# Performance work log

Measured on AMD Instinct MI355X. Metric: run time of the kernel, lower is better.

Reference implementation:

```python
import jax, jax.numpy as jnp
import numpy as np
import math

B, S, D, H = 2, 2048, 1024, 16
HD = D // H  # 64


def setup_inputs() -> dict:
    key = jax.random.key(0)
    ks = jax.random.split(key, 7)
    scale = 1.0 / math.sqrt(D)
    return {
        "hidden_states": jax.random.normal(ks[0], (B, S, D), jnp.float32),
        "attention_mask": jnp.zeros((B, 1, 1, S), jnp.int32),  # 0 = valid (code negates .bool())
        "Wq": jax.random.normal(ks[1], (D, D), jnp.float32) * scale,
        "bq": jnp.zeros((D,), jnp.float32),
        "Wk": jax.random.normal(ks[2], (D, D), jnp.float32) * scale,
        "bk": jnp.zeros((D,), jnp.float32),
        "Wv": jax.random.normal(ks[3], (D, D), jnp.float32) * scale,
        "bv": jnp.zeros((D,), jnp.float32),
    }


def reference(hidden_states, attention_mask, Wq, bq, Wk, bk, Wv, bv):
    b, s, d = hidden_states.shape

    def proj(W, bias):
        # torch Linear: x @ W.T + b ; weight shape [out, in]
        y = jnp.einsum('bsd,ed->bse', hidden_states, W) + bias
        return y.reshape(b, s, H, HD).transpose(0, 2, 1, 3)  # b h s d

    q, k, v = proj(Wq, bq), proj(Wk, bk), proj(Wv, bv)

    scores = jnp.einsum('bhqd,bhkd->bhqk', q, k) * (1.0 / math.sqrt(HD))
    causal = jnp.tril(jnp.ones((s, s), bool))[None, None]          # [1,1,S,S]
    pad = ~(attention_mask.astype(bool))                           # [B,1,1,S], True = valid
    mask = causal & pad
    scores = jnp.where(mask, scores, -jnp.inf)
    probs = jax.nn.softmax(scores, axis=-1)  # dropout prob = 0.0 -> identity
    out = jnp.einsum('bhqk,bhkd->bhqd', probs, v)
    return out.transpose(0, 2, 1, 3).reshape(b, s, d)
```

## Files before the change

### kernel.cpp

```cpp
#include <hip/hip_runtime.h>

typedef __bf16 bf16;
typedef __bf16 bf16x4 __attribute__((ext_vector_type(4)));
typedef __bf16 bf16x8 __attribute__((ext_vector_type(8)));
typedef float f32x4 __attribute__((ext_vector_type(4)));
typedef float f32x16 __attribute__((ext_vector_type(16)));
typedef unsigned u32x4 __attribute__((ext_vector_type(4)));

#define DEV __device__ __forceinline__

typedef const __attribute__((address_space(1))) void gvoid_t;
typedef __attribute__((address_space(3))) void lvoid_t;

DEV void gload_lds16(const void* g, void* l) {
  __builtin_amdgcn_global_load_lds((gvoid_t*)g, (lvoid_t*)l, 16, 0, 0);
}

DEV f32x4 mfma16(bf16x8 a, bf16x8 b, f32x4 c) {
  return __builtin_amdgcn_mfma_f32_16x16x32_bf16(a, b, c, 0, 0, 0);
}
DEV f32x16 mfma32(bf16x8 a, bf16x8 b, f32x16 c) {
  return __builtin_amdgcn_mfma_f32_32x32x16_bf16(a, b, c, 0, 0, 0);
}

DEV unsigned pk2(float lo, float hi) {
  unsigned r;
  asm("v_cvt_pk_bf16_f32 %0, %1, %2" : "=v"(r) : "v"(lo), "v"(hi));
  return r;
}

#define QSCALE 0.18033688011112042f

__global__ __launch_bounds__(256) void cvt_all(
    const float* __restrict__ hs, const float* __restrict__ Wq,
    const float* __restrict__ Wk, const float* __restrict__ Wv,
    bf16* __restrict__ Xb, bf16* __restrict__ Wb) {
  const int i = blockIdx.x * 256 + threadIdx.x;
  const float* src;
  bf16* dst;
  int off;
  if (i < 1048576) {
    src = hs; dst = Xb; off = i;
  } else {
    const int j = i - 1048576;
    const int sel = j >> 18;
    off = j & 262143;
    src = (sel == 0) ? Wq : (sel == 1) ? Wk : Wv;
    dst = Wb + (size_t)sel * 1048576;
  }
  float4 f = reinterpret_cast<const float4*>(src)[off];
  bf16x4 o;
  o[0] = (bf16)f.x; o[1] = (bf16)f.y; o[2] = (bf16)f.z; o[3] = (bf16)f.w;
  reinterpret_cast<bf16x4*>(dst)[off] = o;
}

__global__ __launch_bounds__(256) void gemm_qkv(
    const bf16* __restrict__ X, const bf16* __restrict__ W,
    const float* __restrict__ bq, const float* __restrict__ bk,
    const float* __restrict__ bv,
    bf16* __restrict__ Q, bf16* __restrict__ Kb, bf16* __restrict__ Vt) {
  __shared__ bf16 As[128 * 64];
  __shared__ bf16 Bs[128 * 64];
  const int t = threadIdx.x;
  const int lane = t & 63, w = t >> 6;
  const int wr = w >> 1, wc = w & 1;
  const int bid = blockIdx.x;
  const int swzb = (bid & 7) * 96 + (bid >> 3);
  const int m0 = (swzb / 24) * 128;
  const int n0 = (swzb % 24) * 128;
  const int cl = lane & 15, g8 = (lane >> 4) * 8;

  f32x4 acc[4][4];
  for (int mi = 0; mi < 4; ++mi)
    for (int ni = 0; ni < 4; ++ni)
      for (int r = 0; r < 4; ++r) acc[mi][ni][r] = 0.0f;

  for (int k0 = 0; k0 < 1024; k0 += 64) {
#pragma unroll
    for (int i = 0; i < 4; ++i) {
      int c = i * 256 + t;
      int row = c >> 3, col8 = (c & 7) * 8;
      gload_lds16(X + (size_t)(m0 + row) * 1024 + k0 + col8, As + c * 8);
      gload_lds16(W + (size_t)(n0 + row) * 1024 + k0 + col8, Bs + c * 8);
    }
    __syncthreads();
#pragma unroll
    for (int kk = 0; kk < 64; kk += 32) {
      bf16x8 a[4], b[4];
#pragma unroll
      for (int mi = 0; mi < 4; ++mi)
        a[mi] = *(const bf16x8*)&As[(wr * 64 + mi * 16 + cl) * 64 + kk + g8];
#pragma unroll
      for (int ni = 0; ni < 4; ++ni)
        b[ni] = *(const bf16x8*)&Bs[(wc * 64 + ni * 16 + cl) * 64 + kk + g8];
      __builtin_amdgcn_s_setprio(1);
#pragma unroll
      for (int mi = 0; mi < 4; ++mi)
#pragma unroll
        for (int ni = 0; ni < 4; ++ni)
          acc[mi][ni] = mfma16(a[mi], b[ni], acc[mi][ni]);
      __builtin_amdgcn_s_setprio(0);
    }
    __syncthreads();
  }

  const int rq = (lane >> 4) * 4;
#pragma unroll
  for (int mi = 0; mi < 4; ++mi) {
#pragma unroll
    for (int ni = 0; ni < 4; ++ni) {
      const int n = n0 + wc * 64 + ni * 16 + cl;
      const int mbase = m0 + wr * 64 + mi * 16 + rq;
      const int b = mbase >> 11, s0 = mbase & 2047;
      if (n < 1024) {
        const float bias = bq[n];
        const int h = n >> 6, hd = n & 63;
#pragma unroll
        for (int r = 0; r < 4; ++r)
          Q[(((size_t)(b * 16 + h)) * 2048 + s0 + r) * 64 + hd] =
              (bf16)((acc[mi][ni][r] + bias) * QSCALE);
      } else if (n < 2048) {
        const int n2 = n - 1024;
        const float bias = bk[n2];
        const int h = n2 >> 6, hd = n2 & 63;
#pragma unroll
        for (int r = 0; r < 4; ++r)
          Kb[(((size_t)(b * 16 + h)) * 2048 + s0 + r) * 64 + hd] =
              (bf16)(acc[mi][ni][r] + bias);
      } else {
        const int n2 = n - 2048;
        const float bias = bv[n2];
        const int h = n2 >> 6, hd = n2 & 63;
        bf16x4 pk;
#pragma unroll
        for (int r = 0; r < 4; ++r) pk[r] = (bf16)(acc[mi][ni][r] + bias);
        *(bf16x4*)&Vt[(((size_t)(b * 16 + h)) * 64 + hd) * 2048 + s0] = pk;
      }
    }
  }
}

__global__ __launch_bounds__(512, 4) void flash_attn(
    const bf16* __restrict__ Q, const bf16* __restrict__ K,
    const bf16* __restrict__ Vt, const int* __restrict__ amask,
    float* __restrict__ out) {
  __shared__ __align__(16) char arena[65536];
  __shared__ unsigned long long mk[32];
  bf16* Karena = (bf16*)arena;
  bf16* Varena = (bf16*)(arena + 32768);
  const int t = threadIdx.x, lane = t & 63, w = t >> 6;
  const int bh = blockIdx.x & 31;
  const int p = blockIdx.x >> 5;
  const int b = bh >> 4, h = bh & 15;
  const int g = w >> 1, par = w & 1;
  const int qt = (g < 2) ? (31 - p) : p;
  const int row0 = qt * 64 + (g & 1) * 32;
  const int r31 = lane & 31, hi = lane >> 5;
  const int swz = (r31 & 15) << 4;
  const int ntb = 32 - p;
  const int nsuper = (ntb + 1) >> 1;

  const bf16* Qp = Q + (size_t)bh * 2048 * 64;
  const bf16* Kp = K + (size_t)bh * 2048 * 64;
  const bf16* Vp = Vt + (size_t)bh * 64 * 2048;

  bf16x8 qf[4];
#pragma unroll
  for (int hdk = 0; hdk < 4; ++hdk)
    qf[hdk] = *(const bf16x8*)&Qp[(size_t)(row0 + r31) * 64 + hdk * 16 + hi * 8];

  f32x16 o[2];
#pragma unroll
  for (int hb = 0; hb < 2; ++hb)
#pragma unroll
    for (int rg = 0; rg < 16; ++rg) o[hb][rg] = 0.0f;
  float ls = 0.0f;

#pragma unroll
  for (int i = 0; i < 4; ++i) {
    const int kt = w * 4 + i;
    const unsigned long long bal =
        __ballot(amask[b * 2048 + kt * 64 + lane] != 0);
    if (lane == 0) mk[kt] = bal;
  }
#define STAGE(BIDX, KVB)                                                     \
  do {                                                                       \
    const int r_ = t >> 4, u_ = (t & 15) ^ (r_ & 15);                        \
    const int rr_ = (u_ >> 3) * 32 + r_, gb_ = (u_ & 7) * 8;                 \
    gload_lds16(Kp + (size_t)((KVB) + rr_) * 64 + gb_,                       \
                Karena + (BIDX)*4096 + t * 8);                               \
    gload_lds16(Vp + (size_t)rr_ * 2048 + (KVB) + gb_,                       \
                Varena + (BIDX)*4096 + t * 8);                               \
  } while (0)

  STAGE(0, 0);
  STAGE(1, 64);
  __syncthreads();

  for (int s = 0; s < nsuper; ++s) {
    const int pairbuf = s & 1;
    const int tn = 2 * s + 2;
    if (tn < ntb) STAGE((pairbuf ^ 1) * 2 + 0, tn * 64);
    if (tn + 1 < ntb) STAGE((pairbuf ^ 1) * 2 + 1, (tn + 1) * 64);
    const int kt = 2 * s + par;
    if (kt <= qt) {
      const int kv0 = kt * 64;
      const int bidx = pairbuf * 2 + par;
      const char* KtB = (const char*)(Karena + bidx * 4096);
      const char* VtB = (const char*)(Varena + bidx * 4096);
      const unsigned long long pb = mk[kt];
      const bool diag = (kt == qt);
      const bool domask = diag || (pb != 0ull);
#pragma unroll
      for (int half = 0; half < 2; ++half) {
        f32x16 s4;
#pragma unroll
        for (int rg = 0; rg < 16; ++rg) s4[rg] = -12.0f;
        __builtin_amdgcn_s_setprio(1);
#pragma unroll
        for (int hdk = 0; hdk < 4; ++hdk) {
          const bf16x8 kfr = *(const bf16x8*)(
              KtB + r31 * 256 + ((half * 128 + hdk * 32 + hi * 16) ^ swz));
          s4 = mfma32(kfr, qf[hdk], s4);
        }
        __builtin_amdgcn_s_setprio(0);
        if (domask) {
#pragma unroll
          for (int rg = 0; rg < 16; ++rg) {
            const int kvt = half * 32 + (rg & 3) + 8 * (rg >> 2) + 4 * hi;
            const bool bad = (diag && (kv0 + kvt > row0 + r31)) ||
                             ((pb >> kvt) & 1ull);
            s4[rg] = bad ? -1e30f : s4[rg];
          }
        }
        float pe[16];
#pragma unroll
        for (int rg = 0; rg < 16; ++rg) pe[rg] = exp2f(s4[rg]);
        ls += (((pe[0] + pe[1]) + (pe[2] + pe[3])) +
               ((pe[4] + pe[5]) + (pe[6] + pe[7]))) +
              (((pe[8] + pe[9]) + (pe[10] + pe[11])) +
               ((pe[12] + pe[13]) + (pe[14] + pe[15])));
#pragma unroll
        for (int j = 0; j < 2; ++j) {
          const unsigned a0 = pk2(pe[8 * j + 0], pe[8 * j + 1]);
          const unsigned a1 = pk2(pe[8 * j + 2], pe[8 * j + 3]);
          const unsigned b0 = pk2(pe[8 * j + 4], pe[8 * j + 5]);
          const unsigned b1 = pk2(pe[8 * j + 6], pe[8 * j + 7]);
          const unsigned xa0 = __shfl_xor(a0, 32, 64);
          const unsigned xa1 = __shfl_xor(a1, 32, 64);
          const unsigned xb0 = __shfl_xor(b0, 32, 64);
          const unsigned xb1 = __shfl_xor(b1, 32, 64);
          u32x4 wv;
          wv[0] = hi ? xb0 : a0;
          wv[1] = hi ? xb1 : a1;
          wv[2] = hi ? b0 : xa0;
          wv[3] = hi ? b1 : xa1;
          const bf16x8 paf = __builtin_bit_cast(bf16x8, wv);
          const int kvb = half * 64 + j * 32;
          const bf16x8 vf0 = *(const bf16x8*)(
              VtB + r31 * 256 + ((kvb + hi * 16) ^ swz));
          const bf16x8 vf1 = *(const bf16x8*)(
              VtB + r31 * 256 + ((128 + kvb + hi * 16) ^ swz));
          __builtin_amdgcn_s_setprio(1);
          o[0] = mfma32(paf, vf0, o[0]);
          o[1] = mfma32(paf, vf1, o[1]);
          __builtin_amdgcn_s_setprio(0);
        }
      }
    }
    __syncthreads();
  }

  ls += __shfl_xor(ls, 32, 64);
  float* Op = (float*)arena;
  float* Lp = (float*)(arena + 32768);
  if (par == 1) {
    float* Og = Op + g * 2048;
#pragma unroll
    for (int rg = 0; rg < 16; ++rg) {
      const int qrel = (rg & 3) + 8 * (rg >> 2) + 4 * hi;
      Og[qrel * 64 + r31] = o[0][rg];
      Og[qrel * 64 + 32 + r31] = o[1][rg];
    }
    if (lane < 32) Lp[g * 32 + r31] = ls;
  }
  __syncthreads();
  if (par == 0) {
    const float lt = ls + Lp[g * 32 + r31];
    const float inv = 1.0f / lt;
    const float* Og = Op + g * 2048;
#pragma unroll
    for (int rg = 0; rg < 16; ++rg) {
      const int qrel = (rg & 3) + 8 * (rg >> 2) + 4 * hi;
      const float invq = __shfl(inv, qrel, 64);
      float* op = &out[((size_t)b * 2048 + row0 + qrel) * 1024 + h * 64 + r31];
      op[0] = (o[0][rg] + Og[qrel * 64 + r31]) * invq;
      op[32] = (o[1][rg] + Og[qrel * 64 + 32 + r31]) * invq;
    }
  }
}

extern "C" void kernel_launch(void* const* d_in, const int* in_sizes, int n_in,
                              void* d_out, int out_size, void* d_ws,
                              size_t ws_size, hipStream_t stream) {
  const float* hs = (const float*)d_in[0];
  const int* amask = (const int*)d_in[1];
  const float* Wq = (const float*)d_in[2];
  const float* bq = (const float*)d_in[3];
  const float* Wk = (const float*)d_in[4];
  const float* bk = (const float*)d_in[5];
  const float* Wv = (const float*)d_in[6];
  const float* bv = (const float*)d_in[7];
  float* out = (float*)d_out;

  char* ws = (char*)d_ws;
  bf16* Xb = (bf16*)ws;
  bf16* Wb = (bf16*)(ws + 8ull * 1024 * 1024);
  bf16* Qb = (bf16*)(ws + 14ull * 1024 * 1024);
  bf16* Kb = (bf16*)(ws + 22ull * 1024 * 1024);
  bf16* Vtb = (bf16*)(ws + 30ull * 1024 * 1024);

  cvt_all<<<7168, 256, 0, stream>>>(hs, Wq, Wk, Wv, Xb, Wb);
  gemm_qkv<<<768, 256, 0, stream>>>(Xb, Wb, bq, bk, bv, Qb, Kb, Vtb);
  flash_attn<<<512, 512, 0, stream>>>(Qb, Kb, Vtb, amask, out);
}
```

Baseline: 106.3 us.

## Store K/V in MFMA fragment layout and load directly to registers

```diff
diff --git a/kernel.cpp b/kernel.cpp
--- a/kernel.cpp
+++ b/kernel.cpp
@@ -58,7 +58,7 @@
     const bf16* __restrict__ X, const bf16* __restrict__ W,
     const float* __restrict__ bq, const float* __restrict__ bk,
     const float* __restrict__ bv,
-    bf16* __restrict__ Q, bf16* __restrict__ Kb, bf16* __restrict__ Vt) {
+    bf16* __restrict__ Q, bf16* __restrict__ Kf, bf16* __restrict__ Vf) {
   __shared__ bf16 As[128 * 64];
   __shared__ bf16 Bs[128 * 64];
   const int t = threadIdx.x;
@@ -123,94 +123,84 @@
         const int n2 = n - 1024;
         const float bias = bk[n2];
         const int h = n2 >> 6, hd = n2 & 63;
+        const int kt = s0 >> 6, half = (s0 >> 5) & 1, rr = s0 & 31;
+        const size_t base =
+            ((size_t)((b * 16 + h) * 32 + kt) * 8 + half * 4 + (hd >> 4)) * 512 +
+            ((((hd >> 3) & 1) * 32 + rr) * 8 + (hd & 7));
 #pragma unroll
         for (int r = 0; r < 4; ++r)
-          Kb[(((size_t)(b * 16 + h)) * 2048 + s0 + r) * 64 + hd] =
-              (bf16)(acc[mi][ni][r] + bias);
+          Kf[base + r * 8] = (bf16)(acc[mi][ni][r] + bias);
       } else {
         const int n2 = n - 2048;
         const float bias = bv[n2];
         const int h = n2 >> 6, hd = n2 & 63;
+        const int kt = s0 >> 6, half = (s0 >> 5) & 1;
+        const int j = (s0 >> 4) & 1, hi2 = (s0 >> 3) & 1;
+        const size_t idx =
+            ((size_t)(((b * 16 + h) * 32 + kt) * 4 + half * 2 + j) * 2 +
+             (hd >> 5)) * 512 +
+            ((hi2 * 32 + (hd & 31)) * 8 + (s0 & 7));
         bf16x4 pk;
 #pragma unroll
         for (int r = 0; r < 4; ++r) pk[r] = (bf16)(acc[mi][ni][r] + bias);
-        *(bf16x4*)&Vt[(((size_t)(b * 16 + h)) * 64 + hd) * 2048 + s0] = pk;
+        *(bf16x4*)&Vf[idx] = pk;
       }
     }
   }
 }
 
-__global__ __launch_bounds__(512, 4) void flash_attn(
-    const bf16* __restrict__ Q, const bf16* __restrict__ K,
-    const bf16* __restrict__ Vt, const int* __restrict__ amask,
+__global__ __launch_bounds__(256, 3) void flash_attn(
+    const bf16* __restrict__ Q, const bf16* __restrict__ Kf,
+    const bf16* __restrict__ Vf, const int* __restrict__ amask,
     float* __restrict__ out) {
-  __shared__ __align__(16) char arena[65536];
+  __shared__ float Oar[2][2048];
+  __shared__ float Lar[2][32];
   __shared__ unsigned long long mk[32];
-  bf16* Karena = (bf16*)arena;
-  bf16* Varena = (bf16*)(arena + 32768);
   const int t = threadIdx.x, lane = t & 63, w = t >> 6;
   const int bh = blockIdx.x & 31;
   const int p = blockIdx.x >> 5;
   const int b = bh >> 4, h = bh & 15;
-  const int g = w >> 1, par = w & 1;
-  const int qt = (g < 2) ? (31 - p) : p;
-  const int row0 = qt * 64 + (g & 1) * 32;
+  const int sub = w >> 1, par = w & 1;
   const int r31 = lane & 31, hi = lane >> 5;
-  const int swz = (r31 & 15) << 4;
-  const int ntb = 32 - p;
-  const int nsuper = (ntb + 1) >> 1;
 
   const bf16* Qp = Q + (size_t)bh * 2048 * 64;
-  const bf16* Kp = K + (size_t)bh * 2048 * 64;
-  const bf16* Vp = Vt + (size_t)bh * 64 * 2048;
-
-  bf16x8 qf[4];
-#pragma unroll
-  for (int hdk = 0; hdk < 4; ++hdk)
-    qf[hdk] = *(const bf16x8*)&Qp[(size_t)(row0 + r31) * 64 + hdk * 16 + hi * 8];
-
-  f32x16 o[2];
-#pragma unroll
-  for (int hb = 0; hb < 2; ++hb)
-#pragma unroll
-    for (int rg = 0; rg < 16; ++rg) o[hb][rg] = 0.0f;
-  float ls = 0.0f;
-
-#pragma unroll
-  for (int i = 0; i < 4; ++i) {
-    const int kt = w * 4 + i;
+  const bf16* Kfb = Kf + (size_t)bh * 32 * 4096 + lane * 8;
+  const bf16* Vfb = Vf + (size_t)bh * 32 * 4096 + lane * 8;
+
+#pragma unroll
+  for (int i = 0; i < 8; ++i) {
+    const int kt = w * 8 + i;
     const unsigned long long bal =
         __ballot(amask[b * 2048 + kt * 64 + lane] != 0);
     if (lane == 0) mk[kt] = bal;
   }
-#define STAGE(BIDX, KVB)                                                     \
-  do {                                                                       \
-    const int r_ = t >> 4, u_ = (t & 15) ^ (r_ & 15);                        \
-    const int rr_ = (u_ >> 3) * 32 + r_, gb_ = (u_ & 7) * 8;                 \
-    gload_lds16(Kp + (size_t)((KVB) + rr_) * 64 + gb_,                       \
-                Karena + (BIDX)*4096 + t * 8);                               \
-    gload_lds16(Vp + (size_t)rr_ * 2048 + (KVB) + gb_,                       \
-                Varena + (BIDX)*4096 + t * 8);                               \
-  } while (0)
-
-  STAGE(0, 0);
-  STAGE(1, 64);
   __syncthreads();
 
-  for (int s = 0; s < nsuper; ++s) {
-    const int pairbuf = s & 1;
-    const int tn = 2 * s + 2;
-    if (tn < ntb) STAGE((pairbuf ^ 1) * 2 + 0, tn * 64);
-    if (tn + 1 < ntb) STAGE((pairbuf ^ 1) * 2 + 1, (tn + 1) * 64);
-    const int kt = 2 * s + par;
-    if (kt <= qt) {
-      const int kv0 = kt * 64;
-      const int bidx = pairbuf * 2 + par;
-      const char* KtB = (const char*)(Karena + bidx * 4096);
-      const char* VtB = (const char*)(Varena + bidx * 4096);
+  for (int sw = 0; sw < 2; ++sw) {
+    const int qt = sw ? p : 31 - p;
+    const int row0 = qt * 64 + sub * 32;
+    bf16x8 qf[4];
+#pragma unroll
+    for (int hdk = 0; hdk < 4; ++hdk)
+      qf[hdk] =
+          *(const bf16x8*)&Qp[(size_t)(row0 + r31) * 64 + hdk * 16 + hi * 8];
+    f32x16 o0, o1;
+#pragma unroll
+    for (int rg = 0; rg < 16; ++rg) { o0[rg] = 0.0f; o1[rg] = 0.0f; }
+    float ls = 0.0f;
+
+    for (int kt = par; kt <= qt; kt += 2) {
+      const bf16* kb = Kfb + (size_t)kt * 4096;
+      const bf16* vb = Vfb + (size_t)kt * 4096;
+      bf16x8 kf[8], vf[8];
+#pragma unroll
+      for (int u = 0; u < 8; ++u) kf[u] = *(const bf16x8*)(kb + u * 512);
+#pragma unroll
+      for (int u = 0; u < 8; ++u) vf[u] = *(const bf16x8*)(vb + u * 512);
       const unsigned long long pb = mk[kt];
       const bool diag = (kt == qt);
       const bool domask = diag || (pb != 0ull);
+      const int kv0 = kt * 64;
 #pragma unroll
       for (int half = 0; half < 2; ++half) {
         f32x16 s4;
@@ -218,11 +208,8 @@
         for (int rg = 0; rg < 16; ++rg) s4[rg] = -12.0f;
         __builtin_amdgcn_s_setprio(1);
 #pragma unroll
-        for (int hdk = 0; hdk < 4; ++hdk) {
-          const bf16x8 kfr = *(const bf16x8*)(
-              KtB + r31 * 256 + ((half * 128 + hdk * 32 + hi * 16) ^ swz));
-          s4 = mfma32(kfr, qf[hdk], s4);
-        }
+        for (int hdk = 0; hdk < 4; ++hdk)
+          s4 = mfma32(kf[half * 4 + hdk], qf[hdk], s4);
         __builtin_amdgcn_s_setprio(0);
         if (domask) {
 #pragma unroll
@@ -256,47 +243,41 @@
           wv[2] = hi ? b0 : xa0;
           wv[3] = hi ? b1 : xa1;
           const bf16x8 paf = __builtin_bit_cast(bf16x8, wv);
-          const int kvb = half * 64 + j * 32;
-          const bf16x8 vf0 = *(const bf16x8*)(
-              VtB + r31 * 256 + ((kvb + hi * 16) ^ swz));
-          const bf16x8 vf1 = *(const bf16x8*)(
-              VtB + r31 * 256 + ((128 + kvb + hi * 16) ^ swz));
           __builtin_amdgcn_s_setprio(1);
-          o[0] = mfma32(paf, vf0, o[0]);
-          o[1] = mfma32(paf, vf1, o[1]);
+          o0 = mfma32(paf, vf[half * 4 + j * 2 + 0], o0);
+          o1 = mfma32(paf, vf[half * 4 + j * 2 + 1], o1);
           __builtin_amdgcn_s_setprio(0);
         }
       }
     }
+
+    ls += __shfl_xor(ls, 32, 64);
+    if (par == 1) {
+      float* Og = Oar[sub];
+#pragma unroll
+      for (int rg = 0; rg < 16; ++rg) {
+        const int qrel = (rg & 3) + 8 * (rg >> 2) + 4 * hi;
+        Og[qrel * 64 + r31] = o0[rg];
+        Og[qrel * 64 + 32 + r31] = o1[rg];
+      }
+      if (lane < 32) Lar[sub][r31] = ls;
+    }
     __syncthreads();
-  }
-
-  ls += __shfl_xor(ls, 32, 64);
-  float* Op = (float*)arena;
-  float* Lp = (float*)(arena + 32768);
-  if (par == 1) {
-    float* Og = Op + g * 2048;
-#pragma unroll
-    for (int rg = 0; rg < 16; ++rg) {
-      const int qrel = (rg & 3) + 8 * (rg >> 2) + 4 * hi;
-      Og[qrel * 64 + r31] = o[0][rg];
-      Og[qrel * 64 + 32 + r31] = o[1][rg];
-    }
-    if (lane < 32) Lp[g * 32 + r31] = ls;
-  }
-  __syncthreads();
-  if (par == 0) {
-    const float lt = ls + Lp[g * 32 + r31];
-    const float inv = 1.0f / lt;
-    const float* Og = Op + g * 2048;
-#pragma unroll
-    for (int rg = 0; rg < 16; ++rg) {
-      const int qrel = (rg & 3) + 8 * (rg >> 2) + 4 * hi;
-      const float invq = __shfl(inv, qrel, 64);
-      float* op = &out[((size_t)b * 2048 + row0 + qrel) * 1024 + h * 64 + r31];
-      op[0] = (o[0][rg] + Og[qrel * 64 + r31]) * invq;
-      op[32] = (o[1][rg] + Og[qrel * 64 + 32 + r31]) * invq;
-    }
+    if (par == 0) {
+      const float lt = ls + Lar[sub][r31];
+      const float inv = 1.0f / lt;
+      const float* Og = Oar[sub];
+#pragma unroll
+      for (int rg = 0; rg < 16; ++rg) {
+        const int qrel = (rg & 3) + 8 * (rg >> 2) + 4 * hi;
+        const float invq = __shfl(inv, qrel, 64);
+        float* op =
+            &out[((size_t)b * 2048 + row0 + qrel) * 1024 + h * 64 + r31];
+        op[0] = (o0[rg] + Og[qrel * 64 + r31]) * invq;
+        op[32] = (o1[rg] + Og[qrel * 64 + 32 + r31]) * invq;
+      }
+    }
+    __syncthreads();
   }
 }
 
@@ -317,10 +298,10 @@
   bf16* Xb = (bf16*)ws;
   bf16* Wb = (bf16*)(ws + 8ull * 1024 * 1024);
   bf16* Qb = (bf16*)(ws + 14ull * 1024 * 1024);
-  bf16* Kb = (bf16*)(ws + 22ull * 1024 * 1024);
-  bf16* Vtb = (bf16*)(ws + 30ull * 1024 * 1024);
+  bf16* Kfr = (bf16*)(ws + 22ull * 1024 * 1024);
+  bf16* Vfr = (bf16*)(ws + 30ull * 1024 * 1024);
 
   cvt_all<<<7168, 256, 0, stream>>>(hs, Wq, Wk, Wv, Xb, Wb);
-  gemm_qkv<<<768, 256, 0, stream>>>(Xb, Wb, bq, bk, bv, Qb, Kb, Vtb);
-  flash_attn<<<512, 512, 0, stream>>>(Qb, Kb, Vtb, amask, out);
-}
+  gemm_qkv<<<768, 256, 0, stream>>>(Xb, Wb, bq, bk, bv, Qb, Kfr, Vfr);
+  flash_attn<<<512, 256, 0, stream>>>(Qb, Kfr, Vfr, amask, out);
+}
```

New measurement: 109.7 us. 3.1% more time.
